# Kernel optimization log

Measured on AMD Instinct MI355X. Metric: run time of the kernel, lower is better.

The kernel has to match this reference:

```python
import jax, jax.numpy as jnp
import numpy as np

INPUT_SIZE = 256
HIDDEN_SIZE = 1024
OUTPUT_SIZE = 256


def setup_inputs() -> dict:
    key = jax.random.key(0)
    k_x, k_ih, k_hh, k_fw, k_fb = jax.random.split(key, 5)
    B, S = 64, 512
    x = jax.random.normal(k_x, (B, S, INPUT_SIZE), dtype=jnp.float32)
    weight_ih = jax.random.normal(k_ih, (HIDDEN_SIZE, INPUT_SIZE), dtype=jnp.float32) * 0.01
    weight_hh = jax.random.normal(k_hh, (HIDDEN_SIZE, HIDDEN_SIZE), dtype=jnp.float32) * 0.01
    bias = jnp.zeros((HIDDEN_SIZE,), dtype=jnp.float32)
    # fc layer (nn.Linear default init approximated with uniform)
    lim = 1.0 / np.sqrt(HIDDEN_SIZE)
    fc_w = jax.random.uniform(k_fw, (OUTPUT_SIZE, HIDDEN_SIZE), dtype=jnp.float32, minval=-lim, maxval=lim)
    fc_b = jax.random.uniform(k_fb, (OUTPUT_SIZE,), dtype=jnp.float32, minval=-lim, maxval=lim)
    return {"x": x, "weight_ih": weight_ih, "weight_hh": weight_hh, "bias": bias, "fc_w": fc_w, "fc_b": fc_b}


def reference(x, weight_ih, weight_hh, bias, fc_w, fc_b):
    # x: [B, S, I]
    B = x.shape[0]
    h0 = jnp.zeros((B, weight_hh.shape[0]), dtype=x.dtype)
    # precompute input projections for all timesteps: [S, B, H]
    x_proj = jnp.einsum('bsi,hi->sbh', x, weight_ih)

    def step(h, xp_t):
        h_new = jnp.tanh(xp_t + h @ weight_hh.T + bias)
        return h_new, h_new

    h_last, hs = jax.lax.scan(step, h0, x_proj)
    hidden_states = jnp.concatenate([h0[None], hs], axis=0)  # [S+1, B, H]
    output = h_last @ fc_w.T + fc_b  # [B, O]
    return output, hidden_states
```

## Files before the change

### kernel.cpp

```cpp
#include <hip/hip_runtime.h>
#include <hip/hip_bf16.h>
#include <math.h>

#define B_ 64
#define S_ 512
#define I_ 256
#define H_ 1024
#define O_ 256

#define OUT_OFF (B_*O_)
#define SLOT    (B_*H_)

typedef __attribute__((ext_vector_type(8))) short bf16x8;
typedef __attribute__((ext_vector_type(4))) float f32x4;

#define LDSK 1032

__global__ void k_zero(float* __restrict__ hid, float* __restrict__ hbf0) {
    int i = blockIdx.x * 256 + threadIdx.x;
    ((float4*)hid)[i] = make_float4(0.f, 0.f, 0.f, 0.f);
    if (i < B_ * H_ * 2 / 16)
        ((float4*)hbf0)[i] = make_float4(0.f, 0.f, 0.f, 0.f);
}

__global__ void k_cvt(const float* __restrict__ src, unsigned short* __restrict__ dst) {
    int i = blockIdx.x * 256 + threadIdx.x;
    float4 v = ((const float4*)src)[i];
    ushort4 o;
    o.x = __builtin_bit_cast(unsigned short, __float2bfloat16(v.x));
    o.y = __builtin_bit_cast(unsigned short, __float2bfloat16(v.y));
    o.z = __builtin_bit_cast(unsigned short, __float2bfloat16(v.z));
    o.w = __builtin_bit_cast(unsigned short, __float2bfloat16(v.w));
    ((ushort4*)dst)[i] = o;
}

__global__ void k_transpose(const float* __restrict__ src, float* __restrict__ dst,
                            int R, int C) {
    __shared__ float tile[32][33];
    int c0 = blockIdx.x * 32, r0 = blockIdx.y * 32;
    int tx = threadIdx.x, ty = threadIdx.y;
#pragma unroll
    for (int j = 0; j < 32; j += 8)
        tile[ty + j][tx] = src[(size_t)(r0 + ty + j) * C + c0 + tx];
    __syncthreads();
#pragma unroll
    for (int j = 0; j < 32; j += 8)
        dst[(size_t)(c0 + ty + j) * R + r0 + tx] = tile[tx][ty + j];
}

__global__ __launch_bounds__(256) void k_xproj(const float* __restrict__ x,
                                               const float* __restrict__ wihT,
                                               const float* __restrict__ bias,
                                               float* __restrict__ hid) {
    const int t   = blockIdx.x;
    const int hq0 = blockIdx.y * 16;
    __shared__ float xs[B_][260];
    const int tid = threadIdx.x;

#pragma unroll
    for (int it = 0; it < 16; ++it) {
        int f4 = it * 256 + tid;
        int b = f4 >> 6, iq = f4 & 63;
        float4 v = ((const float4*)x)[(size_t)b * (S_ * I_ / 4) + t * (I_ / 4) + iq];
        *(float4*)&xs[b][iq * 4] = v;
    }
    __syncthreads();

    const int hq = tid & 15;
    const int b0 = (tid >> 4) * 4;
    float4 acc[4];
    float4 bs = ((const float4*)bias)[hq0 + hq];
#pragma unroll
    for (int i = 0; i < 4; ++i) acc[i] = bs;

    const float4* w4p = (const float4*)wihT;
#pragma unroll 4
    for (int k = 0; k < I_; ++k) {
        float4 w = w4p[(size_t)k * (H_ / 4) + hq0 + hq];
#pragma unroll
        for (int i = 0; i < 4; ++i) {
            float xv = xs[b0 + i][k];
            acc[i].x += xv * w.x; acc[i].y += xv * w.y;
            acc[i].z += xv * w.z; acc[i].w += xv * w.w;
        }
    }

    float4* out4 = (float4*)hid;
#pragma unroll
    for (int i = 0; i < 4; ++i)
        out4[(size_t)(t + 1) * (SLOT / 4) + (b0 + i) * (H_ / 4) + hq0 + hq] = acc[i];
}

__global__ __launch_bounds__(256) void k_step(
    const unsigned short* __restrict__ whhbf,
    const unsigned short* __restrict__ hprev,
    unsigned short* __restrict__ hnext,
    float* __restrict__ hid, int t)
{
    const int slice = blockIdx.x;
    __shared__ unsigned short Ws[16 * LDSK];
    const int tid = threadIdx.x;

    {
        const float4* src = (const float4*)(whhbf + (size_t)slice * 16 * H_);
#pragma unroll
        for (int it = 0; it < 8; ++it) {
            int c = it * 256 + tid;
            float4 v = src[c];
            int row = c >> 7, off = (c & 127) * 8;
            *(float4*)&Ws[row * LDSK + off] = v;
        }
    }
    __syncthreads();

    const int w    = tid >> 6;
    const int lane = tid & 63;
    const int n    = lane & 15;
    const int quad = lane >> 4;

    const int b = w * 16 + n;
    f32x4 acc = {0.f, 0.f, 0.f, 0.f};

    const unsigned short* ap = &Ws[n * LDSK + quad * 8];
    const unsigned short* bp = hprev + (size_t)b * H_ + quad * 8;

#pragma unroll
    for (int kk = 0; kk < 32; ++kk) {
        bf16x8 af = *(const bf16x8*)(ap + kk * 32);
        bf16x8 bf = *(const bf16x8*)(bp + kk * 32);
        acc = __builtin_amdgcn_mfma_f32_16x16x32_bf16(af, bf, acc, 0, 0, 0);
    }

    const int r0 = slice * 16 + quad * 4;
    float4* slot1 = (float4*)(hid + (size_t)(t + 1) * SLOT);
    size_t idx = (size_t)b * (H_ / 4) + (r0 >> 2);
    float4 xp = slot1[idx];
    float4 hv;
    hv.x = tanhf(acc[0] + xp.x);
    hv.y = tanhf(acc[1] + xp.y);
    hv.z = tanhf(acc[2] + xp.z);
    hv.w = tanhf(acc[3] + xp.w);
    slot1[idx] = hv;

    ushort4 hb;
    hb.x = __builtin_bit_cast(unsigned short, __float2bfloat16(hv.x));
    hb.y = __builtin_bit_cast(unsigned short, __float2bfloat16(hv.y));
    hb.z = __builtin_bit_cast(unsigned short, __float2bfloat16(hv.z));
    hb.w = __builtin_bit_cast(unsigned short, __float2bfloat16(hv.w));
    *(ushort4*)(hnext + (size_t)b * H_ + r0) = hb;
}

__global__ __launch_bounds__(256) void k_fc(const float* __restrict__ fcwT,
                                            const float* __restrict__ fcb,
                                            const float* __restrict__ hid,
                                            float* __restrict__ outp) {
    const int b = blockIdx.x;
    __shared__ float hl[H_];
    const int tid = threadIdx.x;
    ((float4*)hl)[tid] = ((const float4*)(hid + (size_t)S_ * SLOT + b * H_))[tid];
    __syncthreads();
    float acc = fcb[tid];
#pragma unroll 4
    for (int k = 0; k < H_; ++k)
        acc += fcwT[(size_t)k * O_ + tid] * hl[k];
    outp[b * O_ + tid] = acc;
}

extern "C" void kernel_launch(void* const* d_in, const int* in_sizes, int n_in,
                              void* d_out, int out_size, void* d_ws, size_t ws_size,
                              hipStream_t stream) {
    const float* x    = (const float*)d_in[0];
    const float* wih  = (const float*)d_in[1];
    const float* whh  = (const float*)d_in[2];
    const float* bias = (const float*)d_in[3];
    const float* fcw  = (const float*)d_in[4];
    const float* fcb  = (const float*)d_in[5];

    float* outp = (float*)d_out;
    float* hid  = outp + OUT_OFF;

    unsigned short* whhbf = (unsigned short*)d_ws;
    unsigned short* hbf0  = whhbf + (size_t)H_ * H_;
    unsigned short* hbf1  = hbf0 + (size_t)B_ * H_;
    float* wihT = (float*)(hbf1 + (size_t)B_ * H_);
    float* fcwT = wihT + (size_t)I_ * H_;

    k_zero<<<SLOT / 4 / 256, 256, 0, stream>>>(hid, (float*)hbf0);
    k_cvt<<<H_ * H_ / 4 / 256, 256, 0, stream>>>(whh, whhbf);
    k_transpose<<<dim3(I_ / 32, H_ / 32), dim3(32, 8), 0, stream>>>(wih, wihT, H_, I_);
    k_transpose<<<dim3(H_ / 32, O_ / 32), dim3(32, 8), 0, stream>>>(fcw, fcwT, O_, H_);

    k_xproj<<<dim3(S_, H_ / 64), 256, 0, stream>>>(x, wihT, bias, hid);

    unsigned short* hp[2] = {hbf0, hbf1};
    for (int t = 0; t < S_; ++t)
        k_step<<<64, 256, 0, stream>>>(whhbf, hp[t & 1], hp[(t + 1) & 1], hid, t);

    k_fc<<<B_, 256, 0, stream>>>(fcwT, fcb, hid, outp);
}
```

Baseline: 3.999 ms.

## Replace per-timestep kernel launches with one persistent cooperative kernel using grid sync

The 512 per-step kernel launches become a single cooperative kernel. Its 64 blocks load their W_hh slice into LDS once and loop over all timesteps, separated by grid.sync(). This removes launch overhead and the repeated per-step weight reload into shared memory. In exchange it depends on grid-wide barrier cost and on cooperative launch support, and hprev is read through __restrict__ pointers that may be cached across iterations, a possible correctness risk.

After: 7.585 ms. 1.9x slower.

```diff
diff --git a/kernel.cpp b/kernel.cpp
--- a/kernel.cpp
+++ b/kernel.cpp
@@ -1,6 +1,9 @@
 #include <hip/hip_runtime.h>
 #include <hip/hip_bf16.h>
+#include <hip/hip_cooperative_groups.h>
 #include <math.h>
+
+namespace cg = cooperative_groups;
 
 #define B_ 64
 #define S_ 512
@@ -91,11 +94,11 @@
         out4[(size_t)(t + 1) * (SLOT / 4) + (b0 + i) * (H_ / 4) + hq0 + hq] = acc[i];
 }
 
-__global__ __launch_bounds__(256) void k_step(
+__global__ __launch_bounds__(256) void k_loop(
     const unsigned short* __restrict__ whhbf,
-    const unsigned short* __restrict__ hprev,
-    unsigned short* __restrict__ hnext,
-    float* __restrict__ hid, int t)
+    unsigned short* __restrict__ hbuf0,
+    unsigned short* __restrict__ hbuf1,
+    float* __restrict__ hid)
 {
     const int slice = blockIdx.x;
     __shared__ unsigned short Ws[16 * LDSK];
@@ -117,37 +120,47 @@
     const int lane = tid & 63;
     const int n    = lane & 15;
     const int quad = lane >> 4;
-
-    const int b = w * 16 + n;
-    f32x4 acc = {0.f, 0.f, 0.f, 0.f};
+    const int b    = w * 16 + n;
 
     const unsigned short* ap = &Ws[n * LDSK + quad * 8];
-    const unsigned short* bp = hprev + (size_t)b * H_ + quad * 8;
-
-#pragma unroll
-    for (int kk = 0; kk < 32; ++kk) {
-        bf16x8 af = *(const bf16x8*)(ap + kk * 32);
-        bf16x8 bf = *(const bf16x8*)(bp + kk * 32);
-        acc = __builtin_amdgcn_mfma_f32_16x16x32_bf16(af, bf, acc, 0, 0, 0);
-    }
-
     const int r0 = slice * 16 + quad * 4;
-    float4* slot1 = (float4*)(hid + (size_t)(t + 1) * SLOT);
-    size_t idx = (size_t)b * (H_ / 4) + (r0 >> 2);
-    float4 xp = slot1[idx];
-    float4 hv;
-    hv.x = tanhf(acc[0] + xp.x);
-    hv.y = tanhf(acc[1] + xp.y);
-    hv.z = tanhf(acc[2] + xp.z);
-    hv.w = tanhf(acc[3] + xp.w);
-    slot1[idx] = hv;
-
-    ushort4 hb;
-    hb.x = __builtin_bit_cast(unsigned short, __float2bfloat16(hv.x));
-    hb.y = __builtin_bit_cast(unsigned short, __float2bfloat16(hv.y));
-    hb.z = __builtin_bit_cast(unsigned short, __float2bfloat16(hv.z));
-    hb.w = __builtin_bit_cast(unsigned short, __float2bfloat16(hv.w));
-    *(ushort4*)(hnext + (size_t)b * H_ + r0) = hb;
+    const size_t didx = (size_t)b * (H_ / 4) + (r0 >> 2);
+    const size_t hoff = (size_t)b * H_;
+
+    cg::grid_group grid = cg::this_grid();
+
+    for (int t = 0; t < S_; ++t) {
+        const unsigned short* hp = (t & 1) ? hbuf1 : hbuf0;
+        unsigned short*       hn = (t & 1) ? hbuf0 : hbuf1;
+        float4* slot1 = (float4*)(hid + (size_t)(t + 1) * SLOT);
+
+        float4 xp = slot1[didx];
+        const unsigned short* bp = hp + hoff + quad * 8;
+
+        f32x4 acc = {0.f, 0.f, 0.f, 0.f};
+#pragma unroll
+        for (int kk = 0; kk < 32; ++kk) {
+            bf16x8 af = *(const bf16x8*)(ap + kk * 32);
+            bf16x8 bf = *(const bf16x8*)(bp + kk * 32);
+            acc = __builtin_amdgcn_mfma_f32_16x16x32_bf16(af, bf, acc, 0, 0, 0);
+        }
+
+        float4 hv;
+        hv.x = tanhf(acc[0] + xp.x);
+        hv.y = tanhf(acc[1] + xp.y);
+        hv.z = tanhf(acc[2] + xp.z);
+        hv.w = tanhf(acc[3] + xp.w);
+        slot1[didx] = hv;
+
+        ushort4 hb;
+        hb.x = __builtin_bit_cast(unsigned short, __float2bfloat16(hv.x));
+        hb.y = __builtin_bit_cast(unsigned short, __float2bfloat16(hv.y));
+        hb.z = __builtin_bit_cast(unsigned short, __float2bfloat16(hv.z));
+        hb.w = __builtin_bit_cast(unsigned short, __float2bfloat16(hv.w));
+        *(ushort4*)(hn + hoff + r0) = hb;
+
+        grid.sync();
+    }
 }
 
 __global__ __launch_bounds__(256) void k_fc(const float* __restrict__ fcwT,
@@ -192,9 +205,10 @@
 
     k_xproj<<<dim3(S_, H_ / 64), 256, 0, stream>>>(x, wihT, bias, hid);
 
-    unsigned short* hp[2] = {hbf0, hbf1};
-    for (int t = 0; t < S_; ++t)
-        k_step<<<64, 256, 0, stream>>>(whhbf, hp[t & 1], hp[(t + 1) & 1], hid, t);
+    {
+        void* args[] = {(void*)&whhbf, (void*)&hbf0, (void*)&hbf1, (void*)&hid};
+        hipLaunchCooperativeKernel((void*)k_loop, dim3(64), dim3(256), args, 0, stream);
+    }
 
     k_fc<<<B_, 256, 0, stream>>>(fcwT, fcb, hid, outp);
 }
```
